# Kernel optimization log

Hardware: AMD Instinct MI355X
Metric: run time of the kernel (lower is better)

## Reference

```python
import jax, jax.numpy as jnp
import numpy as np

IMAGE_SIZE = 128
B = 2048
PI = float(np.pi)


def setup_inputs() -> dict:
    key = jax.random.key(0)
    k1, k2, k3 = jax.random.split(key, 3)
    W = jax.random.normal(k1, (B, 16), dtype=jnp.float32)
    noise_gauss = jax.random.normal(k2, (B, IMAGE_SIZE, IMAGE_SIZE), dtype=jnp.float32)
    noise_uniform = jax.random.uniform(k3, (B, IMAGE_SIZE, IMAGE_SIZE), dtype=jnp.float32)
    return {"W": W, "noise_gauss": noise_gauss, "noise_uniform": noise_uniform}


def _decode(W, noise_gauss, noise_uniform):
    H = IMAGE_SIZE
    cx = cy = H // 2
    xx, yy = jnp.meshgrid(jnp.arange(H, dtype=jnp.float32),
                          jnp.arange(H, dtype=jnp.float32), indexing="ij")  # (H,H)

    def w(k):
        return W[:, k][:, None, None]  # (B,1,1) for broadcasting over pixels

    r = jnp.sqrt((xx - cx) ** 2 + (yy - cy) ** 2)  # (H,H)

    # disk
    img = jnp.clip(w(0) * 6 - r, 0.0, 1.0)  # (B,H,H)

    # central square (mask replaces dynamic slice img[cy-half:cy+half, cx-half:cx+half])
    half = jnp.floor(jnp.clip(jnp.abs(w(1)) * 8 + 2, 2, 12))
    square = ((xx >= cy - half) & (xx < cy + half) &
              (yy >= cx - half) & (yy < cx + half)).astype(jnp.float32)
    img = img + 0.5 * square

    # sinusoids
    img = img + 0.5 * jnp.sin(w(2) * 2 * PI * xx / H)
    img = img + 0.5 * jnp.sin(w(3) * 2 * PI * yy / H)
    diag = (xx + yy) / 2
    img = img + 0.5 * jnp.sin(w(4) * PI * diag / H)
    img = img + 0.5 * jnp.sin((yy + w(5) * 10) * PI / H)

    # brightness offset
    img = img + w(6)

    # gaussian blob (int() truncates toward zero)
    off = jnp.trunc(w(7) * 5)
    bx = cx + off
    by = cy + off
    sigma = 4 + jnp.abs(w(7)) * 5
    img = img + jnp.exp(-((xx - bx) ** 2 + (yy - by) ** 2) / (2 * sigma ** 2))

    # ring
    img = img + ((r - w(8) * 10) ** 2 < 10).astype(jnp.float32)

    # checkerboard
    cb_size = jnp.floor(jnp.clip(jnp.abs(w(9)) * 8 + 2, 2, 16))
    cb = (jnp.floor(xx / cb_size) + jnp.floor(yy / cb_size)) % 2 * 0.3
    img = img + cb

    # rotated line
    angle = w(10) * PI
    rot_line = jnp.cos(angle) * (xx - cx) + jnp.sin(angle) * (yy - cy)
    img = img + (jnp.abs(rot_line) < 3).astype(jnp.float32) * 0.6

    # angular sinusoid
    theta = jnp.arctan2(yy - cy, xx - cx)
    img = img + 0.5 * jnp.sin(theta * w(11) * 4)

    # noise
    img = img + noise_gauss * 0.2 * w(12)
    img = img + (noise_uniform - 0.5) * w(13) * 0.2

    # contrast + optional inversion
    img = (img - 0.5) * (1 + w(14)) + 0.5
    img = jnp.where(w(15) > 0, 1.0 - img, img)

    # per-image min/max normalization
    mn = jnp.min(img, axis=(1, 2), keepdims=True)
    mx = jnp.max(img, axis=(1, 2), keepdims=True)
    img = (img - mn) / (mx - mn + 1e-8)
    return img[:, None, :, :]  # (B,1,H,W)


def reference(W, noise_gauss, noise_uniform):
    return _decode(W, noise_gauss, noise_uniform)
```

## Files before the change

### kernel.cpp

```cpp
#include <hip/hip_runtime.h>

#define IMG_H   128
#define NPIX    (IMG_H * IMG_H)
#define TPB     1024
#define VITERS  (NPIX / (TPB * 4))
#define NWAVES  (TPB / 64)

typedef float vfloat4 __attribute__((ext_vector_type(4)));

__device__ __forceinline__ float fast_atan2f(float y, float x) {
    float ax = fabsf(x), ay = fabsf(y);
    float mx = fmaxf(fmaxf(ax, ay), 1e-30f);
    float mn = fminf(ax, ay);
    float a  = mn * __builtin_amdgcn_rcpf(mx);
    float t  = a * a;
    float r  = fmaf(t, fmaf(t, fmaf(t, fmaf(t, 0.0208351f, -0.0851330f),
                                    0.1801410f), -0.3302995f), 0.9998660f);
    r = a * r;
    if (ay > ax)  r = 1.5707963268f - r;
    if (x < 0.0f) r = 3.1415926536f - r;
    return copysignf(r, y);
}

__global__ __launch_bounds__(256)
void theta_init(float* __restrict__ th) {
    const int p = blockIdx.x * 256 + threadIdx.x;
    const int i = p >> 7, j = p & 127;
    th[p] = fast_atan2f((float)j - 64.0f, (float)i - 64.0f);
}

template<bool USE_TAB>
__global__ __launch_bounds__(TPB)
void decode_kernel(const float* __restrict__ W,
                   const float* __restrict__ ng,
                   const float* __restrict__ nu,
                   const float* __restrict__ th,
                   float* __restrict__ out)
{
    const int b   = blockIdx.x;
    const int tid = threadIdx.x;
    const float* Wb = W + (size_t)b * 16;

    const float w0  = Wb[0],  w1  = Wb[1],  w2  = Wb[2],  w3  = Wb[3];
    const float w4  = Wb[4],  w5  = Wb[5],  w6  = Wb[6],  w7  = Wb[7];
    const float w8  = Wb[8],  w9  = Wb[9],  w10 = Wb[10], w11 = Wb[11];
    const float w12 = Wb[12], w13 = Wb[13], w14 = Wb[14], w15 = Wb[15];

    const float PI    = 3.14159265358979323846f;
    const float PI128 = PI / 128.0f;

    const float cdisk = w0 * 6.0f;
    const float half  = floorf(fminf(fmaxf(fabsf(w1) * 8.0f + 2.0f, 2.0f), 12.0f));
    const float lo    = 64.0f - half, hi = 64.0f + half;
    const float s2    = w2 * (PI / 64.0f);
    const float s3    = w3 * (PI / 64.0f);
    const float s4    = w4 * (PI / 256.0f);
    const float c5    = w5 * 10.0f * PI128;
    const float off7  = truncf(w7 * 5.0f);
    const float bxy   = 64.0f + off7;
    const float sig   = 4.0f + fabsf(w7) * 5.0f;
    const float nb    = -1.0f / (2.0f * sig * sig);
    const float r8    = w8 * 10.0f;
    const float cbs   = floorf(fminf(fmaxf(fabsf(w9) * 8.0f + 2.0f, 2.0f), 16.0f));
    const float icbs  = 1.0f / cbs;
    const float ca    = cosf(w10 * PI);
    const float sa    = sinf(w10 * PI);
    const float a11   = w11 * 4.0f;
    const float n12   = 0.2f * w12;
    const float n13   = 0.2f * w13;
    const float con2  = (w15 > 0.0f) ? -(1.0f + w14) : (1.0f + w14);
    const float ccon  = 0.5f - 0.5f * con2;

    __shared__ float4 colA[IMG_H], colB[IMG_H], rowA[IMG_H], rowB[IMG_H];
    __shared__ float  smin[NWAVES], smax[NWAVES];

    if (tid < 128) {
        const float fj  = (float)tid;
        const float dy  = fj - 64.0f;
        const float dyb = fj - bxy;
        const float c0 = 0.5f * __sinf(s3 * fj)
                       + 0.5f * __sinf(fmaf(fj, PI128, c5))
                       + w6 - 0.5f * n13;
        const float cexp = __expf(nb * dyb * dyb);
        const float csq  = ((fj >= lo) && (fj < hi)) ? 0.5f : 0.0f;
        const float cj   = floorf((fj + 0.25f) * icbs);
        const float cpar = (float)(((int)cj) & 1);
        const int   sw   = tid ^ ((tid >> 3) & 7);
        colA[sw] = make_float4(c0, cexp, csq, cpar);
        colB[sw] = make_float4(0.5f * __sinf(s4 * fj), 0.5f * __cosf(s4 * fj), dy, dy * dy);
    } else if (tid < 256) {
        const int   i   = tid - 128;
        const float fi  = (float)i;
        const float dx  = fi - 64.0f;
        const float dxb = fi - bxy;
        const float mi_f = ((fi >= lo) && (fi < hi)) ? 1.0f : 0.0f;
        const float ci   = floorf((fi + 0.25f) * icbs);
        const float rpar = (float)(((int)ci) & 1);
        rowA[i] = make_float4(dx, dx * dx, __expf(nb * dxb * dxb), mi_f);
        rowB[i] = make_float4(rpar, 0.5f * __sinf(s2 * fi), __sinf(s4 * fi), __cosf(s4 * fi));
    }
    __syncthreads();

    const vfloat4* ng4  = (const vfloat4*)(ng  + (size_t)b * NPIX);
    const vfloat4* nu4  = (const vfloat4*)(nu  + (size_t)b * NPIX);
    const vfloat4* th4  = (const vfloat4*)th;
    vfloat4*       out4 = (vfloat4*)(out + (size_t)b * NPIX);

    const int i0 = tid >> 5;
    const int j0 = (tid & 31) << 2;

    float4 cA[4], cB[4];
    #pragma unroll
    for (int q = 0; q < 4; ++q) {
        const int sw = (j0 + q) ^ ((j0 >> 3) & 7);
        cA[q] = colA[sw];
        cB[q] = colB[sw];
    }

    vfloat4 vals[VITERS];
    float vmin =  3.402823466e38f;
    float vmax = -3.402823466e38f;

    #pragma unroll
    for (int k = 0; k < VITERS; ++k) {
        const int p4 = k * TPB + tid;
        const vfloat4 gc = __builtin_nontemporal_load(ng4 + p4);
        const vfloat4 uc = __builtin_nontemporal_load(nu4 + p4);
        vfloat4 tc;
        if (USE_TAB) tc = th4[p4];

        const int    i  = i0 + 32 * k;
        const float4 ra = rowA[i];
        const float4 rb = rowB[i];
        const float  dx  = ra.x;
        const float  rr  = ca * dx;

        const float gg[4] = {gc.x, gc.y, gc.z, gc.w};
        const float uu[4] = {uc.x, uc.y, uc.z, uc.w};

        float vout[4];
        #pragma unroll
        for (int q = 0; q < 4; ++q) {
            const float dy  = cB[q].z;
            const float r2  = ra.y + cB[q].w;
            const float r   = sqrtf(r2);

            float v = fminf(fmaxf(cdisk - r, 0.0f), 1.0f);
            v += cA[q].x;
            v += rb.y;
            v = fmaf(ra.w, cA[q].z, v);
            v = fmaf(rb.z, cB[q].y, v);
            v = fmaf(rb.w, cB[q].x, v);
            v = fmaf(ra.z, cA[q].y, v);
            const float tr = r - r8;
            if (tr * tr < 10.0f) v += 1.0f;
            v = fmaf(fabsf(rb.x - cA[q].w), 0.3f, v);
            const float rot = fmaf(sa, dy, rr);
            if (fabsf(rot) < 3.0f) v += 0.6f;
            float theta;
            if (USE_TAB) theta = (q == 0) ? tc.x : (q == 1) ? tc.y : (q == 2) ? tc.z : tc.w;
            else         theta = fast_atan2f(dy, dx);
            v = fmaf(0.5f, __sinf(theta * a11), v);
            v = fmaf(gg[q], n12, v);
            v = fmaf(uu[q], n13, v);
            v = fmaf(v, con2, ccon);

            vout[q] = v;
            vmin = fminf(vmin, v);
            vmax = fmaxf(vmax, v);
        }
        vfloat4 vv; vv.x = vout[0]; vv.y = vout[1]; vv.z = vout[2]; vv.w = vout[3];
        vals[k] = vv;
    }

    #pragma unroll
    for (int off = 32; off > 0; off >>= 1) {
        vmin = fminf(vmin, __shfl_xor(vmin, off, 64));
        vmax = fmaxf(vmax, __shfl_xor(vmax, off, 64));
    }

    const int wave = tid >> 6;
    if ((tid & 63) == 0) { smin[wave] = vmin; smax[wave] = vmax; }
    __syncthreads();
    float bmin = smin[0], bmax = smax[0];
    #pragma unroll
    for (int wv = 1; wv < NWAVES; ++wv) {
        bmin = fminf(bmin, smin[wv]);
        bmax = fmaxf(bmax, smax[wv]);
    }

    const float scale = 1.0f / (bmax - bmin + 1e-8f);

    #pragma unroll
    for (int k = 0; k < VITERS; ++k) {
        vfloat4 v = vals[k];
        v.x = (v.x - bmin) * scale;
        v.y = (v.y - bmin) * scale;
        v.z = (v.z - bmin) * scale;
        v.w = (v.w - bmin) * scale;
        __builtin_nontemporal_store(v, out4 + k * TPB + tid);
    }
}

extern "C" void kernel_launch(void* const* d_in, const int* in_sizes, int n_in,
                              void* d_out, int out_size, void* d_ws, size_t ws_size,
                              hipStream_t stream) {
    const float* W  = (const float*)d_in[0];
    const float* ng = (const float*)d_in[1];
    const float* nu = (const float*)d_in[2];
    float* out = (float*)d_out;
    const int B = in_sizes[0] / 16;

    if (ws_size >= NPIX * sizeof(float)) {
        float* th = (float*)d_ws;
        theta_init<<<dim3(NPIX / 256), dim3(256), 0, stream>>>(th);
        decode_kernel<true><<<dim3(B), dim3(TPB), 0, stream>>>(W, ng, nu, th, out);
    } else {
        decode_kernel<false><<<dim3(B), dim3(TPB), 0, stream>>>(W, ng, nu, nullptr, out);
    }
}
```

Before: 314.1 us.

## Precompute radius and normalized angle table, fold contrast into final normalization

```diff
diff --git a/kernel.cpp b/kernel.cpp
--- a/kernel.cpp
+++ b/kernel.cpp
@@ -7,6 +7,8 @@
 #define NWAVES  (TPB / 64)
 
 typedef float vfloat4 __attribute__((ext_vector_type(4)));
+
+#define INV2PI 0.15915494309189535f
 
 __device__ __forceinline__ float fast_atan2f(float y, float x) {
     float ax = fabsf(x), ay = fabsf(y);
@@ -23,14 +25,18 @@
 }
 
 __global__ __launch_bounds__(256)
-void theta_init(float* __restrict__ th) {
+void geom_init(float* __restrict__ th) {
     const int p = blockIdx.x * 256 + threadIdx.x;
     const int i = p >> 7, j = p & 127;
-    th[p] = fast_atan2f((float)j - 64.0f, (float)i - 64.0f);
+    const float dx = (float)i - 64.0f;
+    const float dy = (float)j - 64.0f;
+    const float r2 = fmaf(dx, dx, dy * dy);
+    th[2 * p]     = sqrtf(r2);
+    th[2 * p + 1] = fast_atan2f(dy, dx) * INV2PI;
 }
 
 template<bool USE_TAB>
-__global__ __launch_bounds__(TPB)
+__global__ __launch_bounds__(TPB, 8)
 void decode_kernel(const float* __restrict__ W,
                    const float* __restrict__ ng,
                    const float* __restrict__ nu,
@@ -69,7 +75,6 @@
     const float n12   = 0.2f * w12;
     const float n13   = 0.2f * w13;
     const float con2  = (w15 > 0.0f) ? -(1.0f + w14) : (1.0f + w14);
-    const float ccon  = 0.5f - 0.5f * con2;
 
     __shared__ float4 colA[IMG_H], colB[IMG_H], rowA[IMG_H], rowB[IMG_H];
     __shared__ float  smin[NWAVES], smax[NWAVES];
@@ -97,7 +102,9 @@
         const float ci   = floorf((fi + 0.25f) * icbs);
         const float rpar = (float)(((int)ci) & 1);
         rowA[i] = make_float4(dx, dx * dx, __expf(nb * dxb * dxb), mi_f);
-        rowB[i] = make_float4(rpar, 0.5f * __sinf(s2 * fi), __sinf(s4 * fi), __cosf(s4 * fi));
+        rowB[i] = make_float4(0.3f - 0.6f * rpar,
+                              fmaf(0.5f, __sinf(s2 * fi), 0.3f * rpar),
+                              __sinf(s4 * fi), __cosf(s4 * fi));
     }
     __syncthreads();
 
@@ -124,10 +131,10 @@
     #pragma unroll
     for (int k = 0; k < VITERS; ++k) {
         const int p4 = k * TPB + tid;
-        const vfloat4 gc = __builtin_nontemporal_load(ng4 + p4);
-        const vfloat4 uc = __builtin_nontemporal_load(nu4 + p4);
-        vfloat4 tc;
-        if (USE_TAB) tc = th4[p4];
+        const vfloat4 gc = ng4[p4];
+        const vfloat4 uc = nu4[p4];
+        vfloat4 t01, t23;
+        if (USE_TAB) { t01 = th4[2 * p4]; t23 = th4[2 * p4 + 1]; }
 
         const int    i  = i0 + 32 * k;
         const float4 ra = rowA[i];
@@ -137,13 +144,19 @@
 
         const float gg[4] = {gc.x, gc.y, gc.z, gc.w};
         const float uu[4] = {uc.x, uc.y, uc.z, uc.w};
+        const float rq[4] = {t01.x, t01.z, t23.x, t23.z};
+        const float tq[4] = {t01.y, t01.w, t23.y, t23.w};
 
         float vout[4];
         #pragma unroll
         for (int q = 0; q < 4; ++q) {
-            const float dy  = cB[q].z;
-            const float r2  = ra.y + cB[q].w;
-            const float r   = sqrtf(r2);
+            const float dy = cB[q].z;
+            float r, trev;
+            if (USE_TAB) { r = rq[q]; trev = tq[q]; }
+            else {
+                r    = sqrtf(ra.y + cB[q].w);
+                trev = fast_atan2f(dy, dx) * INV2PI;
+            }
 
             float v = fminf(fmaxf(cdisk - r, 0.0f), 1.0f);
             v += cA[q].x;
@@ -154,21 +167,18 @@
             v = fmaf(ra.z, cA[q].y, v);
             const float tr = r - r8;
             if (tr * tr < 10.0f) v += 1.0f;
-            v = fmaf(fabsf(rb.x - cA[q].w), 0.3f, v);
+            v = fmaf(cA[q].w, rb.x, v);
             const float rot = fmaf(sa, dy, rr);
             if (fabsf(rot) < 3.0f) v += 0.6f;
-            float theta;
-            if (USE_TAB) theta = (q == 0) ? tc.x : (q == 1) ? tc.y : (q == 2) ? tc.z : tc.w;
-            else         theta = fast_atan2f(dy, dx);
-            v = fmaf(0.5f, __sinf(theta * a11), v);
+            v = fmaf(0.5f, __builtin_amdgcn_sinf(trev * a11), v);
             v = fmaf(gg[q], n12, v);
             v = fmaf(uu[q], n13, v);
-            v = fmaf(v, con2, ccon);
 
             vout[q] = v;
-            vmin = fminf(vmin, v);
-            vmax = fmaxf(vmax, v);
         }
+        vmin = fminf(fminf(vout[0], vout[1]), fminf(vout[2], fminf(vout[3], vmin)));
+        vmax = fmaxf(fmaxf(vout[0], vout[1]), fmaxf(vout[2], fmaxf(vout[3], vmax)));
+
         vfloat4 vv; vv.x = vout[0]; vv.y = vout[1]; vv.z = vout[2]; vv.w = vout[3];
         vals[k] = vv;
     }
@@ -189,15 +199,19 @@
         bmax = fmaxf(bmax, smax[wv]);
     }
 
-    const float scale = 1.0f / (bmax - bmin + 1e-8f);
+    const float range = bmax - bmin;
+    const float einv  = 1e-8f / fabsf(con2);
+    const float sc    = 1.0f / (range + einv);
+    const float sfin  = (con2 > 0.0f) ? sc : -sc;
+    const float cfin  = (con2 > 0.0f) ? -bmin * sc : bmax * sc;
 
     #pragma unroll
     for (int k = 0; k < VITERS; ++k) {
         vfloat4 v = vals[k];
-        v.x = (v.x - bmin) * scale;
-        v.y = (v.y - bmin) * scale;
-        v.z = (v.z - bmin) * scale;
-        v.w = (v.w - bmin) * scale;
+        v.x = fmaf(v.x, sfin, cfin);
+        v.y = fmaf(v.y, sfin, cfin);
+        v.z = fmaf(v.z, sfin, cfin);
+        v.w = fmaf(v.w, sfin, cfin);
         __builtin_nontemporal_store(v, out4 + k * TPB + tid);
     }
 }
@@ -211,9 +225,9 @@
     float* out = (float*)d_out;
     const int B = in_sizes[0] / 16;
 
-    if (ws_size >= NPIX * sizeof(float)) {
+    if (ws_size >= 2 * NPIX * sizeof(float)) {
         float* th = (float*)d_ws;
-        theta_init<<<dim3(NPIX / 256), dim3(256), 0, stream>>>(th);
+        geom_init<<<dim3(NPIX / 256), dim3(256), 0, stream>>>(th);
         decode_kernel<true><<<dim3(B), dim3(TPB), 0, stream>>>(W, ng, nu, th, out);
     } else {
         decode_kernel<false><<<dim3(B), dim3(TPB), 0, stream>>>(W, ng, nu, nullptr, out);
```

Result: slower. 354.9 us (+13.0%).
